# Performance work log

Measured on AMD Instinct MI355X. Metric: run time of the kernel, lower is better.

Reference implementation:

```python
import jax, jax.numpy as jnp
import numpy as np

B = 8192          # batch_size (pairs of embeddings)
D = 1024          # embedding dim
C = 1024          # number of classes (torch.unique(labels) -> 0..C-1, all present)
EPS = 1e-12       # F.normalize eps


def _normalize(x):
    # F.normalize(x, dim=1): x / max(||x||_2, eps)
    n = jnp.linalg.norm(x, axis=1, keepdims=True)
    return x / jnp.maximum(n, EPS)


def setup_inputs() -> dict:
    key = jax.random.key(0)
    k1, k2, k3 = jax.random.split(key, 3)
    emb_i = jax.random.normal(k1, (B, D), dtype=jnp.float32)
    emb_j = jax.random.normal(k2, (B, D), dtype=jnp.float32)
    # shuffled arange % C guarantees every class id in [0, C) appears,
    # matching torch.unique(labels) == arange(C)
    labels = jax.random.permutation(k3, jnp.arange(B, dtype=jnp.int32) % C).astype(jnp.int64)
    return {"emb_i": emb_i, "emb_j": emb_j, "labels": labels}


def reference(emb_i, emb_j, labels):
    z_i = _normalize(emb_i)  # [B, D]
    z_j = _normalize(emb_j)  # [B, D]

    # vectorized replacement of the per-label python loop:
    # class_prototypes[c] = mean of z_i rows with label c  (segment mean)
    seg_sum = jax.ops.segment_sum(z_i, labels, num_segments=C)                    # [C, D]
    seg_cnt = jax.ops.segment_sum(jnp.ones((B,), z_i.dtype), labels, num_segments=C)  # [C]
    prototypes = seg_sum / seg_cnt[:, None]                                       # [C, D]

    # similarity = 2 - cdist(z_j, prototypes, p=2)
    d2 = (jnp.sum(z_j * z_j, axis=1)[:, None]
          + jnp.sum(prototypes * prototypes, axis=1)[None, :]
          - 2.0 * z_j @ prototypes.T)                                             # [B, C]
    sim = 2.0 - jnp.sqrt(jnp.maximum(d2, 0.0))

    # match_matrix: labels_proto (arange(C)) == labels[:, None]
    match = (jnp.arange(C)[None, :] == labels[:, None]).astype(sim.dtype)         # [B, C]

    # BCEWithLogitsLoss (mean reduction), numerically stable via log_sigmoid
    loss = jnp.mean(-(match * jax.nn.log_sigmoid(sim)
                      + (1.0 - match) * jax.nn.log_sigmoid(-sim)))
    return loss
```

## Files before the change

### kernel.cpp

```cpp
#include <hip/hip_runtime.h>

#define B_N 8192
#define D_N 1024
#define C_N 1024

typedef __attribute__((ext_vector_type(8))) __bf16 bf16x8;
typedef __attribute__((ext_vector_type(4))) float floatx4;

__device__ inline unsigned short f2bf(float f) {
  union { float f; unsigned int u; } cv; cv.f = f;
  unsigned int b = cv.u;
  unsigned int r = (b + 0x7FFFu + ((b >> 16) & 1u)) >> 16;
  return (unsigned short)r;
}
__device__ inline float bf2f(unsigned short u) {
  union { unsigned int u; float f; } cv; cv.u = ((unsigned int)u) << 16;
  return cv.f;
}

__global__ __launch_bounds__(256) void normalize_kernel(
    const float* __restrict__ emb_i, const float* __restrict__ emb_j,
    const int* __restrict__ labels,
    unsigned short* __restrict__ z_i, unsigned short* __restrict__ z_j,
    int* __restrict__ cnt, int* __restrict__ idx) {
  __shared__ float sred[4];
  const int b = blockIdx.x;
  const bool is_i = (b < B_N);
  const int row = is_i ? b : b - B_N;
  const float* src = (is_i ? emb_i : emb_j) + (size_t)row * D_N;

  float4 v = ((const float4*)src)[threadIdx.x];
  float ss = v.x * v.x + v.y * v.y + v.z * v.z + v.w * v.w;
  for (int o = 32; o; o >>= 1) ss += __shfl_xor(ss, o, 64);
  if ((threadIdx.x & 63) == 0) sred[threadIdx.x >> 6] = ss;
  __syncthreads();
  const float tot = sred[0] + sred[1] + sred[2] + sred[3];
  const float inv = 1.0f / fmaxf(sqrtf(tot), 1e-12f);

  ushort4 u;
  u.x = f2bf(v.x * inv); u.y = f2bf(v.y * inv);
  u.z = f2bf(v.z * inv); u.w = f2bf(v.w * inv);
  ((ushort4*)((is_i ? z_i : z_j) + (size_t)row * D_N))[threadIdx.x] = u;

  if (is_i && threadIdx.x == 0) {
    const int lab = labels[row];
    const int pos = atomicAdd(&cnt[lab], 1) & 7;
    idx[lab * 8 + pos] = row;
  }
}

__global__ __launch_bounds__(256) void proto_kernel(
    const unsigned short* __restrict__ z_i, const int* __restrict__ idx,
    unsigned short* __restrict__ proto, float* __restrict__ p2) {
  __shared__ float sred[4];
  __shared__ int sidx[8];
  const int c = blockIdx.x;
  if (threadIdx.x < 8) sidx[threadIdx.x] = idx[c * 8 + threadIdx.x];
  __syncthreads();

  float4 acc = make_float4(0.f, 0.f, 0.f, 0.f);
#pragma unroll
  for (int k = 0; k < 8; ++k) {
    const ushort4 u = ((const ushort4*)(z_i + (size_t)sidx[k] * D_N))[threadIdx.x];
    acc.x += bf2f(u.x); acc.y += bf2f(u.y);
    acc.z += bf2f(u.z); acc.w += bf2f(u.w);
  }
  acc.x *= 0.125f; acc.y *= 0.125f; acc.z *= 0.125f; acc.w *= 0.125f;

  float ss = acc.x * acc.x + acc.y * acc.y + acc.z * acc.z + acc.w * acc.w;
  for (int o = 32; o; o >>= 1) ss += __shfl_xor(ss, o, 64);
  if ((threadIdx.x & 63) == 0) sred[threadIdx.x >> 6] = ss;
  __syncthreads();
  if (threadIdx.x == 0) p2[c] = sred[0] + sred[1] + sred[2] + sred[3];

  ushort4 u;
  u.x = f2bf(acc.x); u.y = f2bf(acc.y); u.z = f2bf(acc.z); u.w = f2bf(acc.w);
  ((ushort4*)(proto + (size_t)c * D_N))[threadIdx.x] = u;
}

#define BM 128
#define BN 128
#define BK 64

__global__ __launch_bounds__(256) void gemm_loss_kernel(
    const unsigned short* __restrict__ Zj,
    const unsigned short* __restrict__ P,
    const float* __restrict__ p2,
    const int* __restrict__ labels,
    float* __restrict__ partial) {
  __shared__ __align__(16) unsigned short As[BM * BK];
  __shared__ __align__(16) unsigned short Bs[BN * BK];
  __shared__ float sred[4];

  const int t = threadIdx.x;
  const int lane = t & 63;
  const int wid = t >> 6;
  const int wm = (wid >> 1) * 64;
  const int wn = (wid & 1) * 64;
  const int bm = blockIdx.x;
  const int bn = blockIdx.y;

  floatx4 acc[4][4];
#pragma unroll
  for (int i = 0; i < 4; ++i)
#pragma unroll
    for (int j = 0; j < 4; ++j)
      acc[i][j] = (floatx4){0.f, 0.f, 0.f, 0.f};

  const int srow = t >> 3;
  const int scol = (((t & 7) ^ (srow & 7)) << 3);
  const unsigned short* Ag = Zj + (size_t)(bm * BM + srow) * D_N + scol;
  const unsigned short* Bg = P + (size_t)(bn * BN + srow) * D_N + scol;
  unsigned short* Al = As + t * 8;
  unsigned short* Bl = Bs + t * 8;

  for (int k0 = 0; k0 < D_N; k0 += BK) {
#pragma unroll
    for (int it = 0; it < 4; ++it) {
      __builtin_amdgcn_global_load_lds(
          (const __attribute__((address_space(1))) void*)(Ag + (size_t)it * 32 * D_N + k0),
          (__attribute__((address_space(3))) void*)(Al + it * 2048), 16, 0, 0);
      __builtin_amdgcn_global_load_lds(
          (const __attribute__((address_space(1))) void*)(Bg + (size_t)it * 32 * D_N + k0),
          (__attribute__((address_space(3))) void*)(Bl + it * 2048), 16, 0, 0);
    }
    __syncthreads();
#pragma unroll
    for (int kk = 0; kk < BK; kk += 32) {
      const int swz = ((((kk >> 3) + (lane >> 4)) ^ (lane & 7)) << 3);
      bf16x8 af[4], bfr[4];
#pragma unroll
      for (int mi = 0; mi < 4; ++mi)
        af[mi] = *(const bf16x8*)(As + (wm + mi * 16 + (lane & 15)) * BK + swz);
#pragma unroll
      for (int ni = 0; ni < 4; ++ni)
        bfr[ni] = *(const bf16x8*)(Bs + (wn + ni * 16 + (lane & 15)) * BK + swz);
#pragma unroll
      for (int mi = 0; mi < 4; ++mi)
#pragma unroll
        for (int ni = 0; ni < 4; ++ni)
          acc[mi][ni] = __builtin_amdgcn_mfma_f32_16x16x32_bf16(af[mi], bfr[ni], acc[mi][ni], 0, 0, 0);
    }
    __syncthreads();
  }

  const int colb = bn * BN + wn + (lane & 15);
  const int rowb = bm * BM + wm + ((lane >> 4) << 2);
  float p2c[4];
#pragma unroll
  for (int ni = 0; ni < 4; ++ni) p2c[ni] = p2[colb + ni * 16];

  float lsum = 0.f;
#pragma unroll
  for (int mi = 0; mi < 4; ++mi) {
#pragma unroll
    for (int r = 0; r < 4; ++r) {
      const int row = rowb + mi * 16 + r;
      const int lab = labels[row];
#pragma unroll
      for (int ni = 0; ni < 4; ++ni) {
        const float dot = acc[mi][ni][r];
        const float d2 = 1.0f + p2c[ni] - 2.0f * dot;
        const float s = 2.0f - sqrtf(fmaxf(d2, 0.0f));
        const float sp = fmaxf(s, 0.0f) + log1pf(expf(-fabsf(s)));
        lsum += sp - ((lab == colb + ni * 16) ? s : 0.0f);
      }
    }
  }
  for (int o = 32; o; o >>= 1) lsum += __shfl_xor(lsum, o, 64);
  if (lane == 0) sred[wid] = lsum;
  __syncthreads();
  if (t == 0) partial[blockIdx.y * 64 + blockIdx.x] = sred[0] + sred[1] + sred[2] + sred[3];
}

__global__ __launch_bounds__(256) void final_reduce_kernel(
    const float* __restrict__ partial, float* __restrict__ out) {
  __shared__ double sred[4];
  const int t = threadIdx.x;
  double v = (double)partial[t] + (double)partial[t + 256];
  for (int o = 32; o; o >>= 1) v += __shfl_xor(v, o, 64);
  if ((t & 63) == 0) sred[t >> 6] = v;
  __syncthreads();
  if (t == 0)
    out[0] = (float)((sred[0] + sred[1] + sred[2] + sred[3]) /
                     ((double)B_N * (double)C_N));
}

extern "C" void kernel_launch(void* const* d_in, const int* in_sizes, int n_in,
                              void* d_out, int out_size, void* d_ws, size_t ws_size,
                              hipStream_t stream) {
  const float* emb_i = (const float*)d_in[0];
  const float* emb_j = (const float*)d_in[1];
  const int* labels = (const int*)d_in[2];
  float* out = (float*)d_out;

  char* ws = (char*)d_ws;
  unsigned short* z_i = (unsigned short*)ws;
  unsigned short* z_j = (unsigned short*)(ws + (size_t)16777216);
  unsigned short* proto = (unsigned short*)(ws + (size_t)33554432);
  float* p2 = (float*)(ws + (size_t)35651584);
  float* partial = (float*)(ws + (size_t)35655680);
  int* cnt = (int*)(ws + (size_t)35659776);
  int* idx = (int*)(ws + (size_t)35663872);

  hipMemsetAsync(cnt, 0, C_N * sizeof(int), stream);
  normalize_kernel<<<dim3(2 * B_N), 256, 0, stream>>>(emb_i, emb_j, labels, z_i, z_j, cnt, idx);
  proto_kernel<<<dim3(C_N), 256, 0, stream>>>(z_i, idx, proto, p2);
  gemm_loss_kernel<<<dim3(B_N / BM, C_N / BN), 256, 0, stream>>>(z_j, proto, p2, labels, partial);
  final_reduce_kernel<<<dim3(1), 256, 0, stream>>>(partial, out);
}
```

Before: 153.4 us.

## Fuse emb_i normalization into prototype kernel and reduce loss via atomics

The z_i normalization no longer runs as a separate pass. The prototype kernel now reads the 8 fp32 emb_i rows per class directly, normalizes them in registers and averages them, so the bf16 z_i intermediate is never written or read back. The final reduce kernel is removed and each GEMM block atomically adds its scaled partial sum into the output, which is zeroed by a memset. This saves a large global write/read and one launch, but the float atomics make the summation order nondeterministic and replace the double-precision final sum.

New measurement: 151.8 us. About the same (-1.1%).

```diff
diff --git a/kernel.cpp b/kernel.cpp
--- a/kernel.cpp
+++ b/kernel.cpp
@@ -13,23 +13,21 @@
   unsigned int r = (b + 0x7FFFu + ((b >> 16) & 1u)) >> 16;
   return (unsigned short)r;
 }
-__device__ inline float bf2f(unsigned short u) {
-  union { unsigned int u; float f; } cv; cv.u = ((unsigned int)u) << 16;
-  return cv.f;
-}
-
-__global__ __launch_bounds__(256) void normalize_kernel(
-    const float* __restrict__ emb_i, const float* __restrict__ emb_j,
-    const int* __restrict__ labels,
-    unsigned short* __restrict__ z_i, unsigned short* __restrict__ z_j,
-    int* __restrict__ cnt, int* __restrict__ idx) {
+
+__global__ __launch_bounds__(256) void normj_idx_kernel(
+    const float* __restrict__ emb_j, const int* __restrict__ labels,
+    unsigned short* __restrict__ z_j, int* __restrict__ cnt,
+    int* __restrict__ idx) {
   __shared__ float sred[4];
-  const int b = blockIdx.x;
-  const bool is_i = (b < B_N);
-  const int row = is_i ? b : b - B_N;
-  const float* src = (is_i ? emb_i : emb_j) + (size_t)row * D_N;
-
-  float4 v = ((const float4*)src)[threadIdx.x];
+  const int row = blockIdx.x;
+
+  if (threadIdx.x == 0) {
+    const int lab = labels[row];
+    const int pos = atomicAdd(&cnt[lab], 1) & 7;
+    idx[lab * 8 + pos] = row;
+  }
+
+  const float4 v = ((const float4*)(emb_j + (size_t)row * D_N))[threadIdx.x];
   float ss = v.x * v.x + v.y * v.y + v.z * v.z + v.w * v.w;
   for (int o = 32; o; o >>= 1) ss += __shfl_xor(ss, o, 64);
   if ((threadIdx.x & 63) == 0) sred[threadIdx.x >> 6] = ss;
@@ -40,41 +38,60 @@
   ushort4 u;
   u.x = f2bf(v.x * inv); u.y = f2bf(v.y * inv);
   u.z = f2bf(v.z * inv); u.w = f2bf(v.w * inv);
-  ((ushort4*)((is_i ? z_i : z_j) + (size_t)row * D_N))[threadIdx.x] = u;
-
-  if (is_i && threadIdx.x == 0) {
-    const int lab = labels[row];
-    const int pos = atomicAdd(&cnt[lab], 1) & 7;
-    idx[lab * 8 + pos] = row;
-  }
+  ((ushort4*)(z_j + (size_t)row * D_N))[threadIdx.x] = u;
 }
 
 __global__ __launch_bounds__(256) void proto_kernel(
-    const unsigned short* __restrict__ z_i, const int* __restrict__ idx,
+    const float* __restrict__ emb_i, const int* __restrict__ idx,
     unsigned short* __restrict__ proto, float* __restrict__ p2) {
-  __shared__ float sred[4];
+  __shared__ float sred[4][8];
+  __shared__ float sinv[8];
   __shared__ int sidx[8];
+  const int t = threadIdx.x;
   const int c = blockIdx.x;
-  if (threadIdx.x < 8) sidx[threadIdx.x] = idx[c * 8 + threadIdx.x];
+  if (t < 8) sidx[t] = idx[c * 8 + t];
+  __syncthreads();
+
+  float4 v[8];
+  float ss[8];
+#pragma unroll
+  for (int k = 0; k < 8; ++k) {
+    v[k] = ((const float4*)(emb_i + (size_t)sidx[k] * D_N))[t];
+    ss[k] = v[k].x * v[k].x + v[k].y * v[k].y + v[k].z * v[k].z + v[k].w * v[k].w;
+  }
+#pragma unroll
+  for (int k = 0; k < 8; ++k)
+    for (int o = 32; o; o >>= 1) ss[k] += __shfl_xor(ss[k], o, 64);
+  if ((t & 63) == 0) {
+#pragma unroll
+    for (int k = 0; k < 8; ++k) sred[t >> 6][k] = ss[k];
+  }
+  __syncthreads();
+  if (t < 8) {
+    const float tot = sred[0][t] + sred[1][t] + sred[2][t] + sred[3][t];
+    sinv[t] = 1.0f / fmaxf(sqrtf(tot), 1e-12f);
+  }
   __syncthreads();
 
   float4 acc = make_float4(0.f, 0.f, 0.f, 0.f);
 #pragma unroll
   for (int k = 0; k < 8; ++k) {
-    const ushort4 u = ((const ushort4*)(z_i + (size_t)sidx[k] * D_N))[threadIdx.x];
-    acc.x += bf2f(u.x); acc.y += bf2f(u.y);
-    acc.z += bf2f(u.z); acc.w += bf2f(u.w);
+    const float iv = sinv[k];
+    acc.x += v[k].x * iv; acc.y += v[k].y * iv;
+    acc.z += v[k].z * iv; acc.w += v[k].w * iv;
   }
   acc.x *= 0.125f; acc.y *= 0.125f; acc.z *= 0.125f; acc.w *= 0.125f;
 
-  float ss = acc.x * acc.x + acc.y * acc.y + acc.z * acc.z + acc.w * acc.w;
-  for (int o = 32; o; o >>= 1) ss += __shfl_xor(ss, o, 64);
-  if ((threadIdx.x & 63) == 0) sred[threadIdx.x >> 6] = ss;
-  __syncthreads();
-  if (threadIdx.x == 0) p2[c] = sred[0] + sred[1] + sred[2] + sred[3];
+  float s2 = acc.x * acc.x + acc.y * acc.y + acc.z * acc.z + acc.w * acc.w;
+  for (int o = 32; o; o >>= 1) s2 += __shfl_xor(s2, o, 64);
+  __syncthreads();
+  if ((t & 63) == 0) sred[t >> 6][0] = s2;
+  __syncthreads();
+  if (t == 0) p2[c] = sred[0][0] + sred[1][0] + sred[2][0] + sred[3][0];
 
   ushort4 u;
-  u.x = f2bf(acc.x); u.y = f2bf(acc.y); u.z = f2bf(acc.z); u.w = f2bf(acc.w);
+  u.x = f2bf(acc.x); u.y = f2bf(acc.y);
+  u.z = f2bf(acc.z); u.w = f2bf(acc.w);
   ((ushort4*)(proto + (size_t)c * D_N))[threadIdx.x] = u;
 }
 
@@ -87,7 +104,7 @@
     const unsigned short* __restrict__ P,
     const float* __restrict__ p2,
     const int* __restrict__ labels,
-    float* __restrict__ partial) {
+    float* __restrict__ out) {
   __shared__ __align__(16) unsigned short As[BM * BK];
   __shared__ __align__(16) unsigned short Bs[BN * BK];
   __shared__ float sred[4];
@@ -170,20 +187,9 @@
   for (int o = 32; o; o >>= 1) lsum += __shfl_xor(lsum, o, 64);
   if (lane == 0) sred[wid] = lsum;
   __syncthreads();
-  if (t == 0) partial[blockIdx.y * 64 + blockIdx.x] = sred[0] + sred[1] + sred[2] + sred[3];
-}
-
-__global__ __launch_bounds__(256) void final_reduce_kernel(
-    const float* __restrict__ partial, float* __restrict__ out) {
-  __shared__ double sred[4];
-  const int t = threadIdx.x;
-  double v = (double)partial[t] + (double)partial[t + 256];
-  for (int o = 32; o; o >>= 1) v += __shfl_xor(v, o, 64);
-  if ((t & 63) == 0) sred[t >> 6] = v;
-  __syncthreads();
   if (t == 0)
-    out[0] = (float)((sred[0] + sred[1] + sred[2] + sred[3]) /
-                     ((double)B_N * (double)C_N));
+    atomicAdd(out, (sred[0] + sred[1] + sred[2] + sred[3]) *
+                       (1.0f / ((float)B_N * (float)C_N)));
 }
 
 extern "C" void kernel_launch(void* const* d_in, const int* in_sizes, int n_in,
@@ -195,17 +201,15 @@
   float* out = (float*)d_out;
 
   char* ws = (char*)d_ws;
-  unsigned short* z_i = (unsigned short*)ws;
-  unsigned short* z_j = (unsigned short*)(ws + (size_t)16777216);
-  unsigned short* proto = (unsigned short*)(ws + (size_t)33554432);
-  float* p2 = (float*)(ws + (size_t)35651584);
-  float* partial = (float*)(ws + (size_t)35655680);
-  int* cnt = (int*)(ws + (size_t)35659776);
-  int* idx = (int*)(ws + (size_t)35663872);
+  unsigned short* z_j = (unsigned short*)ws;
+  unsigned short* proto = (unsigned short*)(ws + (size_t)16777216);
+  float* p2 = (float*)(ws + (size_t)18874368);
+  int* cnt = (int*)(ws + (size_t)18878464);
+  int* idx = (int*)(ws + (size_t)18882560);
 
   hipMemsetAsync(cnt, 0, C_N * sizeof(int), stream);
-  normalize_kernel<<<dim3(2 * B_N), 256, 0, stream>>>(emb_i, emb_j, labels, z_i, z_j, cnt, idx);
-  proto_kernel<<<dim3(C_N), 256, 0, stream>>>(z_i, idx, proto, p2);
-  gemm_loss_kernel<<<dim3(B_N / BM, C_N / BN), 256, 0, stream>>>(z_j, proto, p2, labels, partial);
-  final_reduce_kernel<<<dim3(1), 256, 0, stream>>>(partial, out);
-}
+  hipMemsetAsync(out, 0, sizeof(float), stream);
+  normj_idx_kernel<<<dim3(B_N), 256, 0, stream>>>(emb_j, labels, z_j, cnt, idx);
+  proto_kernel<<<dim3(C_N), 256, 0, stream>>>(emb_i, idx, proto, p2);
+  gemm_loss_kernel<<<dim3(B_N / BM, C_N / BN), 256, 0, stream>>>(z_j, proto, p2, labels, out);
+}
```
